# Performance work log

Hardware: AMD Instinct MI355X
Metric: run time of the kernel (lower is better)

Reference implementation:

```python
import jax, jax.numpy as jnp
import numpy as np

N, E, IN = 50000, 800000, 64
HC, FC1, FC2, FC3, OUT = 96, 256, 128, 64, 8
EPS = 1e-5


def setup_inputs() -> dict:
    key = jax.random.key(0)
    ks = jax.random.split(key, 24)
    def lin(k, fi, fo):
        # kaiming_uniform with relu gain: bound = sqrt(6/fi)
        b = np.sqrt(6.0 / fi)
        return jax.random.uniform(k, (fi, fo), jnp.float32, -b, b)
    inp = {
        'x': jax.random.normal(ks[0], (N, IN), jnp.float32),
        'edge_index': jax.random.randint(ks[1], (2, E), 0, N, jnp.int64),
        'w1': lin(ks[2], IN, HC), 'b1': jnp.zeros((HC,), jnp.float32),
        'g1': jax.random.uniform(ks[3], (HC,), jnp.float32, 0.5, 1.5), 'be1': jax.random.normal(ks[4], (HC,), jnp.float32) * 0.1,
        'w2': lin(ks[5], HC, HC), 'b2': jnp.zeros((HC,), jnp.float32),
        'g2': jax.random.uniform(ks[6], (HC,), jnp.float32, 0.5, 1.5), 'be2': jax.random.normal(ks[7], (HC,), jnp.float32) * 0.1,
        'w3': lin(ks[8], HC, HC), 'b3': jnp.zeros((HC,), jnp.float32),
        'g3': jax.random.uniform(ks[9], (HC,), jnp.float32, 0.5, 1.5), 'be3': jax.random.normal(ks[10], (HC,), jnp.float32) * 0.1,
        'lw1': lin(ks[11], HC, FC1), 'lb1': jnp.zeros((FC1,), jnp.float32),
        'lw2': lin(ks[12], FC1, FC2), 'lb2': jnp.zeros((FC2,), jnp.float32),
        'lw3': lin(ks[13], FC2, FC3), 'lb3': jnp.zeros((FC3,), jnp.float32),
        'lw4': lin(ks[14], FC3, OUT), 'lb4': jnp.zeros((OUT,), jnp.float32),
    }
    return inp


def _gcn(x, w, b, src, dst, norm):
    # GCNConv: out[dst] += norm_e * (x @ w)[src]; then + bias
    h = x @ w
    msg = h[src] * norm[:, None]
    return jax.ops.segment_sum(msg, dst, num_segments=N) + b


def _bn_eval(x, g, be):
    # eval-mode BatchNorm1d with running_mean=0, running_var=1
    return x / jnp.sqrt(1.0 + EPS) * g + be


def reference(x, edge_index, w1, b1, g1, be1, w2, b2, g2, be2, w3, b3, g3, be3,
              lw1, lb1, lw2, lb2, lw3, lb3, lw4, lb4):
    loops = jnp.arange(N, dtype=edge_index.dtype)
    src = jnp.concatenate([edge_index[0], loops])
    dst = jnp.concatenate([edge_index[1], loops])
    deg = jax.ops.segment_sum(jnp.ones_like(src, jnp.float32), dst, num_segments=N)
    dinv = jax.lax.rsqrt(deg)  # deg >= 1 due to self loops
    norm = dinv[src] * dinv[dst]

    h = jax.nn.relu(_bn_eval(_gcn(x, w1, b1, src, dst, norm), g1, be1))
    h = jax.nn.relu(_bn_eval(_gcn(h, w2, b2, src, dst, norm), g2, be2))
    h = jax.nn.relu(_bn_eval(_gcn(h, w3, b3, src, dst, norm), g3, be3))
    h = jax.nn.relu(h @ lw1 + lb1)
    h = jax.nn.relu(h @ lw2 + lb2)
    h = jax.nn.relu(h @ lw3 + lb3)
    return h @ lw4 + lb4
```

## Files before the change

kernel.cpp:

```cpp
#include <hip/hip_runtime.h>


#define GN 50000
#define GE 800000
#define NPART 98
#define PSLOT 9216
#define CHK 2048

typedef __attribute__((ext_vector_type(8))) short bf16x8;
typedef __attribute__((ext_vector_type(4))) float floatx4;
typedef __attribute__((ext_vector_type(2))) float floatx2;
typedef __attribute__((ext_vector_type(4))) unsigned int uintx4;

__device__ __forceinline__ float ar1_b2f(unsigned short h) {
    return __uint_as_float(((unsigned)h) << 16);
}
__device__ __forceinline__ unsigned short ar1_f2b(float f) {
    unsigned u = __float_as_uint(f);
    u = u + 0x7FFFu + ((u >> 16) & 1u);
    return (unsigned short)(u >> 16);
}
__device__ __forceinline__ floatx2 ar1_up2(unsigned w) {
    floatx2 t;
    t[0] = __uint_as_float(w << 16);
    t[1] = __uint_as_float(w & 0xFFFF0000u);
    return t;
}

__device__ __forceinline__ int ar1_det64(const int* ei) {
    int l = (int)threadIdx.x & 63;
    int nz = 0;
#pragma unroll
    for (int k = 0; k < 4; k++)
        nz += (ei[2 * (l + 64 * k) + 1] != 0) ? 1 : 0;
#pragma unroll
    for (int o = 1; o < 64; o <<= 1)
        nz += __shfl_xor(nz, o, 64);
    return (nz < 8) ? 1 : 0;
}
__device__ __forceinline__ int ar1_detf32(const unsigned short* xw) {
    int l = (int)threadIdx.x & 63;
    int c = 0;
#pragma unroll
    for (int k = 0; k < 4; k++) {
        unsigned short w = xw[2 * (l + 64 * k)];
        int ex = (w >> 7) & 0xFF;
        if (w == 0 || (ex >= 90 && ex <= 150)) c++;
    }
#pragma unroll
    for (int o = 1; o < 64; o <<= 1)
        c += __shfl_xor(c, o, 64);
    return (c > 200) ? 0 : 1;
}

struct PackAll {
    const void* src[7];
    unsigned short* dst[7];
    int K[7], M[7], start[8];
};
struct SmallCvt {
    const void* src[4];
    float* dst[4];
    int n[4];
    const void* gb[9];
    float* ss[6];
};

__global__ __launch_bounds__(256)
void Arthur1_16458314678864_kernel(PackAll pa, SmallCvt sc,
                                   const int* __restrict__ ei,
                                   const unsigned short* __restrict__ xw,
                                   int* flagI, int* flagF,
                                   int* __restrict__ gcur,
                                   unsigned int* __restrict__ pairs,
                                   unsigned short* __restrict__ xb,
                                   unsigned short* __restrict__ bufA,
                                   unsigned short* __restrict__ bufB,
                                   float* __restrict__ dinvp) {
    int b = (int)blockIdx.x;
    int tid = (int)threadIdx.x;
    if (b < 391) {
        __shared__ int cnt[NPART], base[NPART], cur[NPART];
        for (int i = tid; i < NPART; i += 256) { cnt[i] = 0; cur[i] = 0; }
        int is64 = ar1_det64(ei);
        __syncthreads();
        int e0 = b * CHK;
        unsigned pk[8]; int q[8];
#pragma unroll
        for (int k = 0; k < 8; k++) {
            int e = e0 + k * 256 + tid;
            q[k] = -1; pk[k] = 0;
            if (e < GE) {
                int s = is64 ? ei[2 * e] : ei[e];
                int d = is64 ? ei[2 * (GE + e)] : ei[GE + e];
                if ((unsigned)s < (unsigned)GN && (unsigned)d < (unsigned)GN) {
                    int qq = d >> 9;
                    q[k] = qq;
                    pk[k] = (unsigned)s | ((unsigned)(d & 511) << 17);
                    atomicAdd(&cnt[qq], 1);
                }
            }
        }
        __syncthreads();
        for (int i = tid; i < NPART; i += 256)
            base[i] = (cnt[i] > 0) ? atomicAdd(&gcur[i], cnt[i]) : 0;
        __syncthreads();
#pragma unroll
        for (int k = 0; k < 8; k++) {
            if (q[k] >= 0) {
                int r = base[q[k]] + atomicAdd(&cur[q[k]], 1);
                if (r < PSLOT) pairs[(size_t)q[k] * PSLOT + r] = pk[k];
            }
        }
    } else if (b < 436) {
        int f = ar1_detf32(xw);
        int frag_g = (b - 391) * 4 + (tid >> 6);
        if (frag_g >= 178) return;
        int w = 0;
        while (w < 6 && frag_g >= pa.start[w + 1]) w++;
        int frag = frag_g - pa.start[w];
        int K = pa.K[w], M = pa.M[w];
        int lane = tid & 63;
        int nch = K >> 5;
        int t = frag / nch, c = frag - t * nch;
        int n = t * 16 + (lane & 15);
        int k0 = c * 32 + (lane >> 4) * 8;
        unsigned short* o = pa.dst[w] + ((size_t)frag * 64 + lane) * 8;
        for (int j = 0; j < 8; j++) {
            unsigned short v = 0;
            if (n < M) {
                int idx = (k0 + j) * M + n;
                v = f ? ar1_f2b(((const float*)pa.src[w])[idx])
                      : ((const unsigned short*)pa.src[w])[idx];
            }
            o[j] = v;
        }
    } else if (b == 436) {
        int f = ar1_detf32(xw);
        int i64 = ar1_det64(ei);
        if (tid == 0) { flagI[0] = i64; flagF[0] = f; dinvp[GN] = 0.f; }
        if (tid < 96) {
            bufA[(size_t)GN * 96 + tid] = 0;
            bufB[(size_t)GN * 96 + tid] = 0;
        }
        if (tid >= 96 && tid < 160) xb[(size_t)GN * 64 + (tid - 96)] = 0;
        const float C = 0.9999950000374997f;
        for (int s = 0; s < 4; s++) {
            for (int i = tid; i < sc.n[s]; i += 256) {
                float v = f ? ((const float*)sc.src[s])[i]
                            : ar1_b2f(((const unsigned short*)sc.src[s])[i]);
                sc.dst[s][i] = v;
            }
        }
        for (int k = 0; k < 3; k++) {
            for (int i = tid; i < 96; i += 256) {
                float bb, g, be;
                if (f) {
                    bb = ((const float*)sc.gb[3 * k + 0])[i];
                    g  = ((const float*)sc.gb[3 * k + 1])[i];
                    be = ((const float*)sc.gb[3 * k + 2])[i];
                } else {
                    bb = ar1_b2f(((const unsigned short*)sc.gb[3 * k + 0])[i]);
                    g  = ar1_b2f(((const unsigned short*)sc.gb[3 * k + 1])[i]);
                    be = ar1_b2f(((const unsigned short*)sc.gb[3 * k + 2])[i]);
                }
                sc.ss[2 * k + 0][i] = C * g;
                sc.ss[2 * k + 1][i] = bb * C * g + be;
            }
        }
    } else {
        int f = ar1_detf32(xw);
        size_t t = (size_t)(b - 437) * 256 + (size_t)tid;
        size_t i0 = t * 8;
        if (i0 < (size_t)GN * 64) {
            bf16x8 o;
            if (f) {
                const float* xf = (const float*)xw;
                floatx4 a = *((const floatx4*)(xf + i0));
                floatx4 c = *((const floatx4*)(xf + i0 + 4));
#pragma unroll
                for (int j = 0; j < 4; j++) {
                    o[j]     = (short)ar1_f2b(a[j]);
                    o[4 + j] = (short)ar1_f2b(c[j]);
                }
            } else {
                o = *((const bf16x8*)(xw + i0));
            }
            *((bf16x8*)(xb + i0)) = o;
        }
    }
}

__global__ __launch_bounds__(256)
void ar1_csr(const unsigned int* __restrict__ pairs, const int* __restrict__ gcur,
             int* __restrict__ csr, int* __restrict__ indeg,
             int* __restrict__ offs, float* __restrict__ dinv,
             unsigned short* __restrict__ xb) {
    __shared__ int ncnt[512], pre[512], cur[512], psum[16], red[256];
    int p = (int)blockIdx.x, tid = (int)threadIdx.x;
    red[tid] = (tid < p && tid < NPART) ? gcur[tid] : 0;
    __syncthreads();
    for (int o = 128; o > 0; o >>= 1) {
        if (tid < o) red[tid] += red[tid + o];
        __syncthreads();
    }
    int gbase = red[0];
    int cntE = gcur[p];
    if (cntE > PSLOT) cntE = PSLOT;
    for (int i = tid; i < 512; i += 256) ncnt[i] = 0;
    __syncthreads();
    const unsigned int* pp = pairs + (size_t)p * PSLOT;
    for (int i = tid; i < cntE; i += 256) atomicAdd(&ncnt[pp[i] >> 17], 1);
    __syncthreads();
    if (tid < 16) {
        int s = 0;
        for (int j = tid * 32; j < tid * 32 + 32; j++) { pre[j] = s; s += ncnt[j]; }
        psum[tid] = s;
    }
    __syncthreads();
    if (tid == 0) {
        int s = 0;
        for (int j = 0; j < 16; j++) { int t = psum[j]; psum[j] = s; s += t; }
    }
    __syncthreads();
    if (tid < 16)
        for (int j = tid * 32; j < tid * 32 + 32; j++) pre[j] += psum[tid];
    __syncthreads();
    for (int j = tid; j < 512; j += 256) {
        cur[j] = pre[j];
        int node = p * 512 + j;
        if (node < GN) {
            indeg[node] = ncnt[j];
            offs[node] = gbase + pre[j];
            dinv[node] = rsqrtf((float)(ncnt[j] + 1));
        }
    }
    __syncthreads();
    for (int i = tid; i < cntE; i += 256) {
        unsigned v = pp[i];
        int r = atomicAdd(&cur[v >> 17], 1);
        csr[gbase + r] = (int)(v & 0x1FFFFu);
    }
    for (int i = tid; i < 512 * 8; i += 256) {
        int j = i >> 3, c = i & 7;
        int node = p * 512 + j;
        if (node < GN) {
            float sc = rsqrtf((float)(ncnt[j] + 1));
            bf16x8 v = *((bf16x8*)(xb + (size_t)node * 64 + c * 8));
#pragma unroll
            for (int jj = 0; jj < 8; jj++)
                v[jj] = (short)ar1_f2b(sc * ar1_b2f((unsigned short)v[jj]));
            *((bf16x8*)(xb + (size_t)node * 64 + c * 8)) = v;
        }
    }
}

__global__ __launch_bounds__(1024, 8)
void ar1_ag64g(const unsigned short* __restrict__ Xb, const int* __restrict__ offs,
               const int* __restrict__ indeg, const int* __restrict__ csr,
               const float* __restrict__ dinv,
               const unsigned short* __restrict__ Bp,
               const float* __restrict__ scale, const float* __restrict__ shift,
               unsigned short* __restrict__ C) {
    __shared__ unsigned short AL[16 * 72];
    int tid = (int)threadIdx.x, wv = tid >> 6, lane = tid & 63;
    int nb = (int)blockIdx.x * 16;
    int node = nb + wv;
    int chunk = lane & 7, eslot = lane >> 3;
    float di = dinv[node];
    int off = offs[node], cnt = indeg[node];

    floatx2 acc2[4];
#pragma unroll
    for (int d = 0; d < 4; d++) acc2[d] = (floatx2){0.f, 0.f};

    for (int base = 0; base < cnt; base += 16) {
        int ss[2];
#pragma unroll
        for (int k = 0; k < 2; k++) {
            int e = base + k * 8 + eslot;
            ss[k] = (e < cnt) ? csr[off + e] : GN;
        }
        uintx4 hh[2];
#pragma unroll
        for (int k = 0; k < 2; k++)
            hh[k] = *((const uintx4*)(Xb + (size_t)ss[k] * 64 + chunk * 8));
#pragma unroll
        for (int k = 0; k < 2; k++)
#pragma unroll
            for (int d = 0; d < 4; d++)
                acc2[d] += ar1_up2(hh[k][d]);
    }
#pragma unroll
    for (int d = 0; d < 4; d++)
#pragma unroll
        for (int c = 0; c < 2; c++) {
            acc2[d][c] += __shfl_xor(acc2[d][c], 8, 64);
            acc2[d][c] += __shfl_xor(acc2[d][c], 16, 64);
            acc2[d][c] += __shfl_xor(acc2[d][c], 32, 64);
        }
    if (eslot == 0) {
        bf16x8 h = *((const bf16x8*)(Xb + (size_t)node * 64 + chunk * 8));
        bf16x8 o;
#pragma unroll
        for (int j = 0; j < 8; j++)
            o[j] = (short)ar1_f2b(di * (acc2[j >> 1][j & 1] +
                                        ar1_b2f((unsigned short)h[j])));
        *((bf16x8*)(AL + (size_t)wv * 72 + chunk * 8)) = o;
    }
    __syncthreads();

    if (wv < 6) {
        int m = lane & 15, quad = lane >> 4, t = wv;
        floatx4 g = (floatx4){0.f, 0.f, 0.f, 0.f};
#pragma unroll
        for (int c = 0; c < 2; c++) {
            bf16x8 a = *((const bf16x8*)(AL + (size_t)m * 72 + c * 32 + quad * 8));
            bf16x8 bfr = *((const bf16x8*)(Bp + ((size_t)(t * 2 + c) * 64 + lane) * 8));
            g = __builtin_amdgcn_mfma_f32_16x16x32_bf16(a, bfr, g, 0, 0, 0);
        }
#pragma unroll
        for (int r = 0; r < 4; r++) {
            int row = nb + quad * 4 + r;
            int col = t * 16 + m;
            float v = g[r] * scale[col] + shift[col];
            C[(size_t)row * 96 + col] = ar1_f2b(dinv[row] * fmaxf(v, 0.f));
        }
    }
}

__global__ __launch_bounds__(1024, 8)
void ar1_ag96g(const unsigned short* __restrict__ H, const int* __restrict__ offs,
               const int* __restrict__ indeg, const int* __restrict__ csr,
               const float* __restrict__ dinv,
               const unsigned short* __restrict__ Bp,
               const float* __restrict__ scale, const float* __restrict__ shift,
               unsigned short* __restrict__ C) {
    __shared__ unsigned short AL[16 * 104];
    int tid = (int)threadIdx.x, wv = tid >> 6, lane = tid & 63;
    int nb = (int)blockIdx.x * 16;
    int node = nb + wv;
    int chunk = lane % 12, eslot = lane / 12;
    float di = dinv[node];
    int off = offs[node], cnt = indeg[node];

    floatx2 acc2[4];
#pragma unroll
    for (int d = 0; d < 4; d++) acc2[d] = (floatx2){0.f, 0.f};

    if (lane < 48) {
        for (int base = 0; base < cnt; base += 16) {
            int ss[4];
#pragma unroll
            for (int k = 0; k < 4; k++) {
                int e = base + k * 4 + eslot;
                ss[k] = (e < cnt) ? csr[off + e] : GN;
            }
            uintx4 hh[4];
#pragma unroll
            for (int k = 0; k < 4; k++)
                hh[k] = *((const uintx4*)(H + (size_t)ss[k] * 96 + chunk * 8));
#pragma unroll
            for (int k = 0; k < 4; k++)
#pragma unroll
                for (int d = 0; d < 4; d++)
                    acc2[d] += ar1_up2(hh[k][d]);
        }
    }
#pragma unroll
    for (int d = 0; d < 4; d++)
#pragma unroll
        for (int c = 0; c < 2; c++) {
            float a1 = __shfl(acc2[d][c], lane + 12, 64);
            float a2 = __shfl(acc2[d][c], lane + 24, 64);
            float a3 = __shfl(acc2[d][c], lane + 36, 64);
            acc2[d][c] += a1 + a2 + a3;
        }
    if (lane < 12) {
        bf16x8 hs = *((const bf16x8*)(H + (size_t)node * 96 + chunk * 8));
        bf16x8 o;
#pragma unroll
        for (int j = 0; j < 8; j++)
            o[j] = (short)ar1_f2b(di * (acc2[j >> 1][j & 1] +
                                        ar1_b2f((unsigned short)hs[j])));
        *((bf16x8*)(AL + (size_t)wv * 104 + chunk * 8)) = o;
    }
    __syncthreads();

    if (wv < 6) {
        int m = lane & 15, quad = lane >> 4, t = wv;
        floatx4 g = (floatx4){0.f, 0.f, 0.f, 0.f};
#pragma unroll
        for (int c = 0; c < 3; c++) {
            bf16x8 a = *((const bf16x8*)(AL + (size_t)m * 104 + c * 32 + quad * 8));
            bf16x8 bfr = *((const bf16x8*)(Bp + ((size_t)(t * 3 + c) * 64 + lane) * 8));
            g = __builtin_amdgcn_mfma_f32_16x16x32_bf16(a, bfr, g, 0, 0, 0);
        }
#pragma unroll
        for (int r = 0; r < 4; r++) {
            int row = nb + quad * 4 + r;
            int col = t * 16 + m;
            float v = g[r] * scale[col] + shift[col];
            C[(size_t)row * 96 + col] = ar1_f2b(dinv[row] * fmaxf(v, 0.f));
        }
    }
}

__global__ __launch_bounds__(1024, 8)
void ar1_agmlp(const unsigned short* __restrict__ H, const int* __restrict__ offs,
               const int* __restrict__ indeg, const int* __restrict__ csr,
               const float* __restrict__ dinv,
               const unsigned short* __restrict__ b2w,
               const float* __restrict__ sc3, const float* __restrict__ sh3,
               const unsigned short* __restrict__ b3,
               const unsigned short* __restrict__ b4,
               const unsigned short* __restrict__ b5,
               const unsigned short* __restrict__ b6,
               const float* __restrict__ lb0, const float* __restrict__ lb1,
               const float* __restrict__ lb2, const float* __restrict__ lb3,
               void* __restrict__ out, const int* __restrict__ f32out) {
    __shared__ unsigned short AL[16 * 104];
    __shared__ unsigned short H0[16 * 104];
    __shared__ unsigned short H1[16 * 264];
    __shared__ unsigned short H2[16 * 136];
    __shared__ unsigned short H3[16 * 72];
    int tid = (int)threadIdx.x, wv = tid >> 6, lane = tid & 63;
    int nb = (int)blockIdx.x * 16;
    int node = nb + wv;
    int m = lane & 15, quad = lane >> 4;

    {
        int chunk = lane % 12, eslot = lane / 12;
        float di = dinv[node];
        int off = offs[node], cnt = indeg[node];
        floatx2 acc2[4];
#pragma unroll
        for (int d = 0; d < 4; d++) acc2[d] = (floatx2){0.f, 0.f};
        if (lane < 48) {
            for (int base = 0; base < cnt; base += 16) {
                int ss[4];
#pragma unroll
                for (int k = 0; k < 4; k++) {
                    int e = base + k * 4 + eslot;
                    ss[k] = (e < cnt) ? csr[off + e] : GN;
                }
                uintx4 hh[4];
#pragma unroll
                for (int k = 0; k < 4; k++)
                    hh[k] = *((const uintx4*)(H + (size_t)ss[k] * 96 + chunk * 8));
#pragma unroll
                for (int k = 0; k < 4; k++)
#pragma unroll
                    for (int d = 0; d < 4; d++)
                        acc2[d] += ar1_up2(hh[k][d]);
            }
        }
#pragma unroll
        for (int d = 0; d < 4; d++)
#pragma unroll
            for (int c = 0; c < 2; c++) {
                float a1 = __shfl(acc2[d][c], lane + 12, 64);
                float a2 = __shfl(acc2[d][c], lane + 24, 64);
                float a3 = __shfl(acc2[d][c], lane + 36, 64);
                acc2[d][c] += a1 + a2 + a3;
            }
        if (lane < 12) {
            bf16x8 hs = *((const bf16x8*)(H + (size_t)node * 96 + chunk * 8));
            bf16x8 o;
#pragma unroll
            for (int j = 0; j < 8; j++)
                o[j] = (short)ar1_f2b(di * (acc2[j >> 1][j & 1] +
                                            ar1_b2f((unsigned short)hs[j])));
            *((bf16x8*)(AL + (size_t)wv * 104 + chunk * 8)) = o;
        }
    }
    __syncthreads();

    if (wv < 6) {
        int t = wv;
        floatx4 g = (floatx4){0.f, 0.f, 0.f, 0.f};
#pragma unroll
        for (int c = 0; c < 3; c++) {
            bf16x8 a = *((const bf16x8*)(AL + (size_t)m * 104 + c * 32 + quad * 8));
            bf16x8 bfr = *((const bf16x8*)(b2w + ((size_t)(t * 3 + c) * 64 + lane) * 8));
            g = __builtin_amdgcn_mfma_f32_16x16x32_bf16(a, bfr, g, 0, 0, 0);
        }
#pragma unroll
        for (int r = 0; r < 4; r++) {
            int col = t * 16 + m;
            float v = g[r] * sc3[col] + sh3[col];
            H0[(quad * 4 + r) * 104 + col] = ar1_f2b(fmaxf(v, 0.f));
        }
    }
    __syncthreads();

    {
        int t = wv;
        floatx4 g = (floatx4){0.f, 0.f, 0.f, 0.f};
#pragma unroll
        for (int c = 0; c < 3; c++) {
            bf16x8 a = *((const bf16x8*)(H0 + (size_t)m * 104 + c * 32 + quad * 8));
            bf16x8 bfr = *((const bf16x8*)(b3 + ((size_t)(t * 3 + c) * 64 + lane) * 8));
            g = __builtin_amdgcn_mfma_f32_16x16x32_bf16(a, bfr, g, 0, 0, 0);
        }
#pragma unroll
        for (int r = 0; r < 4; r++) {
            int col = t * 16 + m;
            H1[(quad * 4 + r) * 264 + col] = ar1_f2b(fmaxf(g[r] + lb0[col], 0.f));
        }
    }
    __syncthreads();

    if (wv < 8) {
        int t = wv;
        floatx4 g = (floatx4){0.f, 0.f, 0.f, 0.f};
#pragma unroll
        for (int c = 0; c < 8; c++) {
            bf16x8 a = *((const bf16x8*)(H1 + (size_t)m * 264 + c * 32 + quad * 8));
            bf16x8 bfr = *((const bf16x8*)(b4 + ((size_t)(t * 8 + c) * 64 + lane) * 8));
            g = __builtin_amdgcn_mfma_f32_16x16x32_bf16(a, bfr, g, 0, 0, 0);
        }
#pragma unroll
        for (int r = 0; r < 4; r++) {
            int col = t * 16 + m;
            H2[(quad * 4 + r) * 136 + col] = ar1_f2b(fmaxf(g[r] + lb1[col], 0.f));
        }
    }
    __syncthreads();

    if (wv < 4) {
        int t = wv;
        floatx4 g = (floatx4){0.f, 0.f, 0.f, 0.f};
#pragma unroll
        for (int c = 0; c < 4; c++) {
            bf16x8 a = *((const bf16x8*)(H2 + (size_t)m * 136 + c * 32 + quad * 8));
            bf16x8 bfr = *((const bf16x8*)(b5 + ((size_t)(t * 4 + c) * 64 + lane) * 8));
            g = __builtin_amdgcn_mfma_f32_16x16x32_bf16(a, bfr, g, 0, 0, 0);
        }
#pragma unroll
        for (int r = 0; r < 4; r++) {
            int col = t * 16 + m;
            H3[(quad * 4 + r) * 72 + col] = ar1_f2b(fmaxf(g[r] + lb2[col], 0.f));
        }
    }
    __syncthreads();

    if (wv == 0) {
        floatx4 g = (floatx4){0.f, 0.f, 0.f, 0.f};
#pragma unroll
        for (int c = 0; c < 2; c++) {
            bf16x8 a = *((const bf16x8*)(H3 + (size_t)m * 72 + c * 32 + quad * 8));
            bf16x8 bfr = *((const bf16x8*)(b6 + ((size_t)c * 64 + lane) * 8));
            g = __builtin_amdgcn_mfma_f32_16x16x32_bf16(a, bfr, g, 0, 0, 0);
        }
        int wf32 = f32out[0];
#pragma unroll
        for (int r = 0; r < 4; r++) {
            int row = nb + quad * 4 + r;
            if (m < 8) {
                float v = g[r] + lb3[m];
                if (wf32) ((float*)out)[(size_t)row * 8 + m] = v;
                else ((unsigned short*)out)[(size_t)row * 8 + m] = ar1_f2b(v);
            }
        }
    }
}

extern "C" void kernel_launch(void* const* d_in, const int* in_sizes, int n_in,
                              void* d_out, int out_size, void* d_ws, size_t ws_size,
                              hipStream_t stream) {
    (void)in_sizes; (void)n_in; (void)out_size;

    char* p = (char*)d_ws;
    unsigned short* bufA = (unsigned short*)p; p += (size_t)(GN + 1) * 96 * 2;
    unsigned short* bufB = (unsigned short*)p; p += (size_t)(GN + 1) * 96 * 2;
    unsigned short* xb   = (unsigned short*)p; p += (size_t)(GN + 1) * 64 * 2;
    unsigned int* pairs = (unsigned int*)p; p += (size_t)NPART * PSLOT * 4;
    int* indeg  = (int*)p;    p += (size_t)GN * 4;
    int* offs   = (int*)p;    p += (size_t)GN * 4;
    float* dinv = (float*)p;  p += (size_t)GN * 4 + 64;
    int* csr    = (int*)p;    p += (size_t)GE * 4;
    int* gcur   = (int*)p;    p += 1024;
    int* flagI  = (int*)p;    p += 1024;
    int* flagF  = (int*)p;    p += 1024;
    unsigned short* bpArena = (unsigned short*)p; p += 91136 * 2;
    float* fArena = (float*)p; p += 2048 * 4;
    size_t need = (size_t)(p - (char*)d_ws);
    if (ws_size < need) {
        hipMemsetAsync(d_out, 0x41, (size_t)GN * 8 * 2, stream);
        return;
    }

    unsigned short* bp[7];
    int bpn[7] = {6144, 9216, 9216, 24576, 32768, 8192, 1024};
    {
        unsigned short* q = bpArena;
        for (int i = 0; i < 7; i++) { bp[i] = q; q += bpn[i]; }
    }

    float* lb[4]; float* ss[6];
    {
        float* q = fArena;
        int ln[4] = {256, 128, 64, 8};
        for (int i = 0; i < 4; i++) { lb[i] = q; q += ln[i]; }
        for (int i = 0; i < 6; i++) { ss[i] = q; q += 96; }
    }

    const int* ei = (const int*)d_in[1];
    const unsigned short* xw = (const unsigned short*)d_in[0];

    hipMemsetAsync(gcur, 0, NPART * 4, stream);
    {
        PackAll pa;
        int wsrc[7] = {2, 6, 10, 14, 16, 18, 20};
        int Ks[7] = {64, 96, 96, 96, 256, 128, 64};
        int Ms[7] = {96, 96, 96, 256, 128, 64, 8};
        int cum = 0;
        for (int i = 0; i < 7; i++) {
            pa.src[i] = d_in[wsrc[i]]; pa.dst[i] = bp[i];
            pa.K[i] = Ks[i]; pa.M[i] = Ms[i];
            pa.start[i] = cum;
            cum += (Ms[i] + 15) / 16 * (Ks[i] / 32);
        }
        pa.start[7] = cum;
        SmallCvt sc;
        int lsrc[4] = {15, 17, 19, 21};
        int ln[4] = {256, 128, 64, 8};
        for (int i = 0; i < 4; i++) { sc.src[i] = d_in[lsrc[i]]; sc.dst[i] = lb[i]; sc.n[i] = ln[i]; }
        int gsrc[9] = {3, 4, 5, 7, 8, 9, 11, 12, 13};
        for (int i = 0; i < 9; i++) sc.gb[i] = d_in[gsrc[i]];
        for (int i = 0; i < 6; i++) sc.ss[i] = ss[i];
        Arthur1_16458314678864_kernel<<<2000, 256, 0, stream>>>(
            pa, sc, ei, xw, flagI, flagF, gcur, pairs, xb, bufA, bufB, dinv);
    }
    ar1_csr<<<NPART, 256, 0, stream>>>(pairs, gcur, csr, indeg, offs, dinv, xb);

    const int FB = GN / 16;

    ar1_ag64g<<<FB, 1024, 0, stream>>>(xb, offs, indeg, csr, dinv,
                                       bp[0], ss[0], ss[1], bufA);
    ar1_ag96g<<<FB, 1024, 0, stream>>>(bufA, offs, indeg, csr, dinv,
                                       bp[1], ss[2], ss[3], bufB);
    ar1_agmlp<<<FB, 1024, 0, stream>>>(bufB, offs, indeg, csr, dinv,
                                       bp[2], ss[4], ss[5],
                                       bp[3], bp[4], bp[5], bp[6],
                                       lb[0], lb[1], lb[2], lb[3], d_out, flagF);
}
```

Baseline: 277.7 us.

## Split fused gather+GEMM kernels into separate gather and GEMM launches

Each layer's kernel used to do the neighbour gather for 16 nodes in a 1024-thread block and then run the MFMA transform in the same block. Now a 256-thread gather kernel (4 nodes per block) writes the aggregated features to new global buffers, and a separate GEMM/MLP kernel reads 16 rows back into LDS. The aim is to get rid of large blocks whose waves sit idle at the barrier behind the slowest node's gather, and to improve occupancy and load balance. The cost is three extra launches and an extra global write and read of the aggregated features per layer.

```diff
diff --git a/kernel.cpp b/kernel.cpp
--- a/kernel.cpp
+++ b/kernel.cpp
@@ -255,17 +255,13 @@
     }
 }
 
-__global__ __launch_bounds__(1024, 8)
-void ar1_ag64g(const unsigned short* __restrict__ Xb, const int* __restrict__ offs,
+__global__ __launch_bounds__(256, 8)
+void ar1_gat64(const unsigned short* __restrict__ Xb, const int* __restrict__ offs,
                const int* __restrict__ indeg, const int* __restrict__ csr,
                const float* __restrict__ dinv,
-               const unsigned short* __restrict__ Bp,
-               const float* __restrict__ scale, const float* __restrict__ shift,
-               unsigned short* __restrict__ C) {
-    __shared__ unsigned short AL[16 * 72];
+               unsigned short* __restrict__ Agg) {
     int tid = (int)threadIdx.x, wv = tid >> 6, lane = tid & 63;
-    int nb = (int)blockIdx.x * 16;
-    int node = nb + wv;
+    int node = (int)blockIdx.x * 4 + wv;
     int chunk = lane & 7, eslot = lane >> 3;
     float di = dinv[node];
     int off = offs[node], cnt = indeg[node];
@@ -306,10 +302,79 @@
         for (int j = 0; j < 8; j++)
             o[j] = (short)ar1_f2b(di * (acc2[j >> 1][j & 1] +
                                         ar1_b2f((unsigned short)h[j])));
-        *((bf16x8*)(AL + (size_t)wv * 72 + chunk * 8)) = o;
-    }
-    __syncthreads();
-
+        *((bf16x8*)(Agg + (size_t)node * 64 + chunk * 8)) = o;
+    }
+}
+
+__global__ __launch_bounds__(256, 8)
+void ar1_gat96(const unsigned short* __restrict__ H, const int* __restrict__ offs,
+               const int* __restrict__ indeg, const int* __restrict__ csr,
+               const float* __restrict__ dinv,
+               unsigned short* __restrict__ Agg) {
+    int tid = (int)threadIdx.x, wv = tid >> 6, lane = tid & 63;
+    int node = (int)blockIdx.x * 4 + wv;
+    int chunk = lane % 12, eslot = lane / 12;
+    float di = dinv[node];
+    int off = offs[node], cnt = indeg[node];
+
+    floatx2 acc2[4];
+#pragma unroll
+    for (int d = 0; d < 4; d++) acc2[d] = (floatx2){0.f, 0.f};
+
+    if (lane < 48) {
+        for (int base = 0; base < cnt; base += 16) {
+            int ss[4];
+#pragma unroll
+            for (int k = 0; k < 4; k++) {
+                int e = base + k * 4 + eslot;
+                ss[k] = (e < cnt) ? csr[off + e] : GN;
+            }
+            uintx4 hh[4];
+#pragma unroll
+            for (int k = 0; k < 4; k++)
+                hh[k] = *((const uintx4*)(H + (size_t)ss[k] * 96 + chunk * 8));
+#pragma unroll
+            for (int k = 0; k < 4; k++)
+#pragma unroll
+                for (int d = 0; d < 4; d++)
+                    acc2[d] += ar1_up2(hh[k][d]);
+        }
+    }
+#pragma unroll
+    for (int d = 0; d < 4; d++)
+#pragma unroll
+        for (int c = 0; c < 2; c++) {
+            float a1 = __shfl(acc2[d][c], lane + 12, 64);
+            float a2 = __shfl(acc2[d][c], lane + 24, 64);
+            float a3 = __shfl(acc2[d][c], lane + 36, 64);
+            acc2[d][c] += a1 + a2 + a3;
+        }
+    if (lane < 12) {
+        bf16x8 hs = *((const bf16x8*)(H + (size_t)node * 96 + chunk * 8));
+        bf16x8 o;
+#pragma unroll
+        for (int j = 0; j < 8; j++)
+            o[j] = (short)ar1_f2b(di * (acc2[j >> 1][j & 1] +
+                                        ar1_b2f((unsigned short)hs[j])));
+        *((bf16x8*)(Agg + (size_t)node * 96 + chunk * 8)) = o;
+    }
+}
+
+__global__ __launch_bounds__(512, 8)
+void ar1_gem1(const unsigned int* __restrict__ Agg, const float* __restrict__ dinv,
+              const unsigned short* __restrict__ Bp,
+              const float* __restrict__ scale, const float* __restrict__ shift,
+              unsigned short* __restrict__ C) {
+    __shared__ unsigned short AL[16 * 72];
+    int tid = (int)threadIdx.x;
+    int nb = (int)blockIdx.x * 16;
+    {
+        int row = tid >> 5, dw = tid & 31;
+        ((unsigned*)AL)[row * 36 + dw] = Agg[(size_t)nb * 32 + tid];
+    }
+    __syncthreads();
+
+    int wv = tid >> 6, lane = tid & 63;
     if (wv < 6) {
         int m = lane & 15, quad = lane >> 4, t = wv;
         floatx4 g = (floatx4){0.f, 0.f, 0.f, 0.f};
@@ -329,64 +394,21 @@
     }
 }
 
-__global__ __launch_bounds__(1024, 8)
-void ar1_ag96g(const unsigned short* __restrict__ H, const int* __restrict__ offs,
-               const int* __restrict__ indeg, const int* __restrict__ csr,
-               const float* __restrict__ dinv,
-               const unsigned short* __restrict__ Bp,
-               const float* __restrict__ scale, const float* __restrict__ shift,
-               unsigned short* __restrict__ C) {
+__global__ __launch_bounds__(512, 8)
+void ar1_gem2(const unsigned int* __restrict__ Agg, const float* __restrict__ dinv,
+              const unsigned short* __restrict__ Bp,
+              const float* __restrict__ scale, const float* __restrict__ shift,
+              unsigned short* __restrict__ C) {
     __shared__ unsigned short AL[16 * 104];
-    int tid = (int)threadIdx.x, wv = tid >> 6, lane = tid & 63;
+    int tid = (int)threadIdx.x;
     int nb = (int)blockIdx.x * 16;
-    int node = nb + wv;
-    int chunk = lane % 12, eslot = lane / 12;
-    float di = dinv[node];
-    int off = offs[node], cnt = indeg[node];
-
-    floatx2 acc2[4];
-#pragma unroll
-    for (int d = 0; d < 4; d++) acc2[d] = (floatx2){0.f, 0.f};
-
-    if (lane < 48) {
-        for (int base = 0; base < cnt; base += 16) {
-            int ss[4];
-#pragma unroll
-            for (int k = 0; k < 4; k++) {
-                int e = base + k * 4 + eslot;
-                ss[k] = (e < cnt) ? csr[off + e] : GN;
-            }
-            uintx4 hh[4];
-#pragma unroll
-            for (int k = 0; k < 4; k++)
-                hh[k] = *((const uintx4*)(H + (size_t)ss[k] * 96 + chunk * 8));
-#pragma unroll
-            for (int k = 0; k < 4; k++)
-#pragma unroll
-                for (int d = 0; d < 4; d++)
-                    acc2[d] += ar1_up2(hh[k][d]);
-        }
-    }
-#pragma unroll
-    for (int d = 0; d < 4; d++)
-#pragma unroll
-        for (int c = 0; c < 2; c++) {
-            float a1 = __shfl(acc2[d][c], lane + 12, 64);
-            float a2 = __shfl(acc2[d][c], lane + 24, 64);
-            float a3 = __shfl(acc2[d][c], lane + 36, 64);
-            acc2[d][c] += a1 + a2 + a3;
-        }
-    if (lane < 12) {
-        bf16x8 hs = *((const bf16x8*)(H + (size_t)node * 96 + chunk * 8));
-        bf16x8 o;
-#pragma unroll
-        for (int j = 0; j < 8; j++)
-            o[j] = (short)ar1_f2b(di * (acc2[j >> 1][j & 1] +
-                                        ar1_b2f((unsigned short)hs[j])));
-        *((bf16x8*)(AL + (size_t)wv * 104 + chunk * 8)) = o;
-    }
-    __syncthreads();
-
+    for (int i = tid; i < 768; i += 512) {
+        int row = i / 48, dw = i - row * 48;
+        ((unsigned*)AL)[row * 52 + dw] = Agg[(size_t)nb * 48 + i];
+    }
+    __syncthreads();
+
+    int wv = tid >> 6, lane = tid & 63;
     if (wv < 6) {
         int m = lane & 15, quad = lane >> 4, t = wv;
         floatx4 g = (floatx4){0.f, 0.f, 0.f, 0.f};
@@ -407,18 +429,16 @@
 }
 
 __global__ __launch_bounds__(1024, 8)
-void ar1_agmlp(const unsigned short* __restrict__ H, const int* __restrict__ offs,
-               const int* __restrict__ indeg, const int* __restrict__ csr,
-               const float* __restrict__ dinv,
-               const unsigned short* __restrict__ b2w,
-               const float* __restrict__ sc3, const float* __restrict__ sh3,
-               const unsigned short* __restrict__ b3,
-               const unsigned short* __restrict__ b4,
-               const unsigned short* __restrict__ b5,
-               const unsigned short* __restrict__ b6,
-               const float* __restrict__ lb0, const float* __restrict__ lb1,
-               const float* __restrict__ lb2, const float* __restrict__ lb3,
-               void* __restrict__ out, const int* __restrict__ f32out) {
+void ar1_mlp(const unsigned int* __restrict__ Agg,
+             const unsigned short* __restrict__ b2w,
+             const float* __restrict__ sc3, const float* __restrict__ sh3,
+             const unsigned short* __restrict__ b3,
+             const unsigned short* __restrict__ b4,
+             const unsigned short* __restrict__ b5,
+             const unsigned short* __restrict__ b6,
+             const float* __restrict__ lb0, const float* __restrict__ lb1,
+             const float* __restrict__ lb2, const float* __restrict__ lb3,
+             void* __restrict__ out, const int* __restrict__ f32out) {
     __shared__ unsigned short AL[16 * 104];
     __shared__ unsigned short H0[16 * 104];
     __shared__ unsigned short H1[16 * 264];
@@ -426,53 +446,11 @@
     __shared__ unsigned short H3[16 * 72];
     int tid = (int)threadIdx.x, wv = tid >> 6, lane = tid & 63;
     int nb = (int)blockIdx.x * 16;
-    int node = nb + wv;
     int m = lane & 15, quad = lane >> 4;
 
-    {
-        int chunk = lane % 12, eslot = lane / 12;
-        float di = dinv[node];
-        int off = offs[node], cnt = indeg[node];
-        floatx2 acc2[4];
-#pragma unroll
-        for (int d = 0; d < 4; d++) acc2[d] = (floatx2){0.f, 0.f};
-        if (lane < 48) {
-            for (int base = 0; base < cnt; base += 16) {
-                int ss[4];
-#pragma unroll
-                for (int k = 0; k < 4; k++) {
-                    int e = base + k * 4 + eslot;
-                    ss[k] = (e < cnt) ? csr[off + e] : GN;
-                }
-                uintx4 hh[4];
-#pragma unroll
-                for (int k = 0; k < 4; k++)
-                    hh[k] = *((const uintx4*)(H + (size_t)ss[k] * 96 + chunk * 8));
-#pragma unroll
-                for (int k = 0; k < 4; k++)
-#pragma unroll
-                    for (int d = 0; d < 4; d++)
-                        acc2[d] += ar1_up2(hh[k][d]);
-            }
-        }
-#pragma unroll
-        for (int d = 0; d < 4; d++)
-#pragma unroll
-            for (int c = 0; c < 2; c++) {
-                float a1 = __shfl(acc2[d][c], lane + 12, 64);
-                float a2 = __shfl(acc2[d][c], lane + 24, 64);
-                float a3 = __shfl(acc2[d][c], lane + 36, 64);
-                acc2[d][c] += a1 + a2 + a3;
-            }
-        if (lane < 12) {
-            bf16x8 hs = *((const bf16x8*)(H + (size_t)node * 96 + chunk * 8));
-            bf16x8 o;
-#pragma unroll
-            for (int j = 0; j < 8; j++)
-                o[j] = (short)ar1_f2b(di * (acc2[j >> 1][j & 1] +
-                                            ar1_b2f((unsigned short)hs[j])));
-            *((bf16x8*)(AL + (size_t)wv * 104 + chunk * 8)) = o;
-        }
+    if (tid < 768) {
+        int row = tid / 48, dw = tid - row * 48;
+        ((unsigned*)AL)[row * 52 + dw] = Agg[(size_t)nb * 48 + tid];
     }
     __syncthreads();
 
@@ -575,6 +553,8 @@
     unsigned short* bufA = (unsigned short*)p; p += (size_t)(GN + 1) * 96 * 2;
     unsigned short* bufB = (unsigned short*)p; p += (size_t)(GN + 1) * 96 * 2;
     unsigned short* xb   = (unsigned short*)p; p += (size_t)(GN + 1) * 64 * 2;
+    unsigned short* agg64 = (unsigned short*)p; p += (size_t)GN * 64 * 2;
+    unsigned short* agg96 = (unsigned short*)p; p += (size_t)GN * 96 * 2;
     unsigned int* pairs = (unsigned int*)p; p += (size_t)NPART * PSLOT * 4;
     int* indeg  = (int*)p;    p += (size_t)GN * 4;
     int* offs   = (int*)p;    p += (size_t)GN * 4;
@@ -635,14 +615,18 @@
     }
     ar1_csr<<<NPART, 256, 0, stream>>>(pairs, gcur, csr, indeg, offs, dinv, xb);
 
-    const int FB = GN / 16;
-
-    ar1_ag64g<<<FB, 1024, 0, stream>>>(xb, offs, indeg, csr, dinv,
-                                       bp[0], ss[0], ss[1], bufA);
-    ar1_ag96g<<<FB, 1024, 0, stream>>>(bufA, offs, indeg, csr, dinv,
-                                       bp[1], ss[2], ss[3], bufB);
-    ar1_agmlp<<<FB, 1024, 0, stream>>>(bufB, offs, indeg, csr, dinv,
-                                       bp[2], ss[4], ss[5],
-                                       bp[3], bp[4], bp[5], bp[6],
-                                       lb[0], lb[1], lb[2], lb[3], d_out, flagF);
-}
+    const int GB = GN / 4;
+    const int CB = GN / 16;
+
+    ar1_gat64<<<GB, 256, 0, stream>>>(xb, offs, indeg, csr, dinv, agg64);
+    ar1_gem1<<<CB, 512, 0, stream>>>((const unsigned*)agg64, dinv,
+                                     bp[0], ss[0], ss[1], bufA);
+    ar1_gat96<<<GB, 256, 0, stream>>>(bufA, offs, indeg, csr, dinv, agg96);
+    ar1_gem2<<<CB, 512, 0, stream>>>((const unsigned*)agg96, dinv,
+                                     bp[1], ss[2], ss[3], bufB);
+    ar1_gat96<<<GB, 256, 0, stream>>>(bufB, offs, indeg, csr, dinv, agg96);
+    ar1_mlp<<<CB, 1024, 0, stream>>>((const unsigned*)agg96,
+                                     bp[2], ss[4], ss[5],
+                                     bp[3], bp[4], bp[5], bp[6],
+                                     lb[0], lb[1], lb[2], lb[3], d_out, flagF);
+}
```

Result: no change. 277.4 us (-0.1%).
